# Kernel tuning notes

Measured on AMD Instinct MI355X. Metric: run time of the kernel, lower is better.

## Reference

```python
import math
import jax, jax.numpy as jnp
import numpy as np

N, B, C, H, K = 1024, 8, 512, 8, 5  # seq len, batch, d_model, heads, near_kth
NEG = -1.0e9


def setup_inputs() -> dict:
    key = jax.random.key(0)
    ks = jax.random.split(key, 10)
    s = 0.02
    return {
        "query": jax.random.normal(ks[0], (N, B, C), jnp.float32),
        "key_t": jax.random.normal(ks[1], (N, B, C), jnp.float32),
        "value": jax.random.normal(ks[2], (N, B, C), jnp.float32),
        "src_position": jax.random.normal(ks[3], (N, B, 3), jnp.float32),
        "tgt_position": jax.random.normal(ks[4], (N, B, 3), jnp.float32),
        # nn.MultiheadAttention params (in_proj split into q/k/v, plus out_proj)
        "Wq": jax.random.normal(ks[5], (C, C), jnp.float32) * s,
        "Wk": jax.random.normal(ks[6], (C, C), jnp.float32) * s,
        "Wv": jax.random.normal(ks[7], (C, C), jnp.float32) * s,
        "bq": jnp.zeros((C,), jnp.float32),
        "bk": jnp.zeros((C,), jnp.float32),
        "bv": jnp.zeros((C,), jnp.float32),
        "Wo": jax.random.normal(ks[8], (C, C), jnp.float32) * s,
        "bo": jnp.zeros((C,), jnp.float32),
    }


def reference(query, key_t, value, src_position, tgt_position,
              Wq, Wk, Wv, bq, bk, bv, Wo, bo):
    # --- 'nearby' positional mask ---------------------------------------
    # dist[b, tgt, src] = ||src_position[src,b] - tgt_position[tgt,b]||^2
    diff = src_position[None, :, :, :] - tgt_position[:, None, :, :]  # (Nt,Ns,B,3)
    dist = jnp.sum(diff * diff, axis=-1).transpose(2, 0, 1)           # (B,Nt,Ns)
    # torch: topk(dist, k=5, dim=1, largest=False) -> 5 nearest TARGETS per source
    _, idx = jax.lax.top_k(-dist.transpose(0, 2, 1), K)               # (B,Ns,K) tgt idx
    mask = jnp.full((B, N, N), NEG, jnp.float32)
    b_i = jnp.arange(B)[:, None, None]
    s_i = jnp.arange(N)[None, :, None]
    mask = mask.at[b_i, idx, s_i].set(0.0)                            # (B,Nt,Ns)

    # --- multihead attention (eval mode, dropout=0) ----------------------
    hd = C // H
    scale = 1.0 / math.sqrt(hd)
    q = ((query @ Wq.T + bq) * scale).reshape(N, B, H, hd)
    k = (key_t @ Wk.T + bk).reshape(N, B, H, hd)
    v = (value @ Wv.T + bv).reshape(N, B, H, hd)
    scores = jnp.einsum('tbhd,sbhd->bhts', q, k) + mask[:, None]      # (B,H,Nt,Ns)
    attn = jax.nn.softmax(scores, axis=-1)
    ctx = jnp.einsum('bhts,sbhd->tbhd', attn, v).reshape(N, B, C)
    out = ctx @ Wo.T + bo                                             # (N,B,C)
    attn_avg = attn.mean(axis=1)                                      # (B,Nt,Ns)
    return out, attn_avg
```

## Files before the change

kernel.cpp:

```cpp
#include <hip/hip_runtime.h>
#include <cstdint>
#include <cstddef>

#define NSEQ 1024
#define BATCH 8
#define CMODEL 512
#define NHEAD 8
#define HDIM 64
#define CAP 64
#define FLTMAX 3.402823466e+38f

typedef short bf16x8 __attribute__((ext_vector_type(8)));
typedef float f32x4 __attribute__((ext_vector_type(4)));
typedef unsigned short ushort8v __attribute__((ext_vector_type(8)));
typedef unsigned short ushort2v __attribute__((ext_vector_type(2)));

__device__ inline unsigned short f2bf(float f) {
    unsigned int u = __builtin_bit_cast(unsigned int, f);
    u += 0x7fffu + ((u >> 16) & 1u);
    return (unsigned short)(u >> 16);
}
__device__ inline float bf2f(unsigned short u) {
    return __builtin_bit_cast(float, (unsigned int)u << 16);
}

#define GLDS16(gsrc, ldst) \
    __builtin_amdgcn_global_load_lds((const __attribute__((address_space(1))) void*)(gsrc), \
                                     (__attribute__((address_space(3))) void*)(ldst), 16, 0, 0)

__global__ __launch_bounds__(256) void prep(const float* __restrict__ w0,
                                            const float* __restrict__ w1,
                                            const float* __restrict__ w2,
                                            const float* __restrict__ w3,
                                            const float* __restrict__ value,
                                            unsigned short* __restrict__ o0,
                                            unsigned short* __restrict__ o1,
                                            unsigned short* __restrict__ o2,
                                            unsigned short* __restrict__ o3,
                                            unsigned int* __restrict__ zp,
                                            float* __restrict__ vm_raw) {
    const int bid = blockIdx.x;
    const int tid = threadIdx.x;
    if (bid < 512) {
        const int idx = bid * 256 + tid;
        const int seg = idx >> 15;
        const int c   = idx & 32767;
        const float* src = seg == 0 ? w0 : seg == 1 ? w1 : seg == 2 ? w2 : w3;
        unsigned short* dst = seg == 0 ? o0 : seg == 1 ? o1 : seg == 2 ? o2 : o3;
        const float4 v0 = *(const float4*)(src + (size_t)c * 8);
        const float4 v1 = *(const float4*)(src + (size_t)c * 8 + 4);
        ushort8v u;
        u[0] = f2bf(v0.x); u[1] = f2bf(v0.y); u[2] = f2bf(v0.z); u[3] = f2bf(v0.w);
        u[4] = f2bf(v1.x); u[5] = f2bf(v1.y); u[6] = f2bf(v1.z); u[7] = f2bf(v1.w);
        *(ushort8v*)(dst + (size_t)c * 8) = u;
        return;
    }
    if (bid < 544) {
        zp[(bid - 512) * 256 + tid] = 0u;
        return;
    }
    const int cb = bid - 544;
    const int b = cb >> 3, cg = cb & 7;
    const int ts = tid >> 6, c = cg * 64 + (tid & 63);
    float s = 0.f;
    for (int i = 0; i < 256; ++i) {
        const int t = ts * 256 + i;
        s += value[((size_t)t * BATCH + b) * CMODEL + c];
    }
    __shared__ float sh[4][64];
    sh[ts][tid & 63] = s;
    __syncthreads();
    if (ts == 0)
        vm_raw[b * CMODEL + c] = sh[0][tid & 63] + sh[1][tid & 63] +
                                 sh[2][tid & 63] + sh[3][tid & 63];
}

__global__ __launch_bounds__(256) void topk_scatter(const float* __restrict__ srcp,
                                                    const float* __restrict__ tgtp,
                                                    int* __restrict__ row_cnt,
                                                    int* __restrict__ row_list,
                                                    const unsigned short* __restrict__ Wv,
                                                    const float* __restrict__ bv,
                                                    const float* __restrict__ vm_raw,
                                                    float* __restrict__ vm) {
    if (blockIdx.x >= 2048) {
        const int bsel = blockIdx.x - 2048;
        const int c0 = threadIdx.x * 2;
        float s0 = 0.f, s1 = 0.f;
        const unsigned short* w0r = Wv + (size_t)c0 * CMODEL;
        const unsigned short* w1r = w0r + CMODEL;
        const float* vr = vm_raw + bsel * CMODEL;
        for (int k = 0; k < CMODEL; ++k) {
            const float v = vr[k];
            s0 += v * bf2f(w0r[k]);
            s1 += v * bf2f(w1r[k]);
        }
        vm[bsel * CMODEL + c0]     = s0 * (1.f / (float)NSEQ) + bv[c0];
        vm[bsel * CMODEL + c0 + 1] = s1 * (1.f / (float)NSEQ) + bv[c0 + 1];
        return;
    }

    const int w = threadIdx.x >> 6, lane = threadIdx.x & 63;
    const int wg = blockIdx.x * 4 + w;
    const int s = wg & 1023, b = wg >> 10;

    const float sx = srcp[((size_t)s * BATCH + b) * 3 + 0];
    const float sy = srcp[((size_t)s * BATCH + b) * 3 + 1];
    const float sz = srcp[((size_t)s * BATCH + b) * 3 + 2];

    float dv[16];
    #pragma unroll
    for (int i = 0; i < 16; ++i) {
        const int t = i * 64 + lane;
        const float dx = tgtp[((size_t)t * BATCH + b) * 3 + 0] - sx;
        const float dy = tgtp[((size_t)t * BATCH + b) * 3 + 1] - sy;
        const float dz = tgtp[((size_t)t * BATCH + b) * 3 + 2] - sz;
        dv[i] = dx * dx + dy * dy + dz * dz;
    }

    #pragma unroll
    for (int k = 0; k < 5; ++k) {
        float bvv = FLTMAX;
        int   bii = 0x7fffffff;
        #pragma unroll
        for (int i = 0; i < 16; ++i) {
            if (dv[i] < bvv) { bvv = dv[i]; bii = i * 64 + lane; }
        }
        #pragma unroll
        for (int off = 1; off < 64; off <<= 1) {
            const float ov = __shfl_xor(bvv, off);
            const int   oi = __shfl_xor(bii, off);
            if (ov < bvv || (ov == bvv && oi < bii)) { bvv = ov; bii = oi; }
        }
        if (lane == (bii & 63)) {
            #pragma unroll
            for (int i = 0; i < 16; ++i)
                if (bii == i * 64 + lane) dv[i] = FLTMAX;
        }
        if (lane == 0) {
            const int pos = atomicAdd(&row_cnt[b * NSEQ + bii], 1);
            if (pos < CAP) row_list[((size_t)b * NSEQ + bii) * CAP + pos] = s;
        }
    }
}

__device__ inline void gemm_fp32A_body(const float* __restrict__ A,
                                       const unsigned short* __restrict__ Wbf,
                                       const float* __restrict__ bias,
                                       unsigned short* __restrict__ outp,
                                       float scale, int m0, int n0) {
    __shared__ __align__(16) unsigned short smem[3 * 8192];
    const int tid = threadIdx.x;
    const int l = tid & 63, w = tid >> 6;
    const int wr = (w >> 1) * 64, wc = (w & 1) * 64;
    const int lr = l & 15, g = l >> 4;

    f32x4 acc[4][4] = {};

    const int rowA = tid >> 2;
    const int slA  = tid & 3;
    const int sw   = (rowA >> 1) & 3;
    const float* aS0 = A + (size_t)(m0 + rowA) * CMODEL + slA * 8;
    const float* aS1 = aS0 + (size_t)64 * CMODEL;
    const int adst0 = rowA * 32 + (slA ^ sw) * 8;
    const int adst1 = adst0 + 64 * 32;
    const unsigned short* bS0 = Wbf + (size_t)(n0 + rowA) * CMODEL + (slA ^ sw) * 8;
    const unsigned short* bS1 = bS0 + (size_t)64 * CMODEL;
    const int wb = w * 512;

    float4 a0, a1, a2, a3;
    auto LOADA = [&](int k0) {
        a0 = *(const float4*)(aS0 + k0); a1 = *(const float4*)(aS0 + k0 + 4);
        a2 = *(const float4*)(aS1 + k0); a3 = *(const float4*)(aS1 + k0 + 4);
    };
    auto CVT_WRITE = [&](int buf) {
        ushort8v u0, u1;
        u0[0] = f2bf(a0.x); u0[1] = f2bf(a0.y); u0[2] = f2bf(a0.z); u0[3] = f2bf(a0.w);
        u0[4] = f2bf(a1.x); u0[5] = f2bf(a1.y); u0[6] = f2bf(a1.z); u0[7] = f2bf(a1.w);
        u1[0] = f2bf(a2.x); u1[1] = f2bf(a2.y); u1[2] = f2bf(a2.z); u1[3] = f2bf(a2.w);
        u1[4] = f2bf(a3.x); u1[5] = f2bf(a3.y); u1[6] = f2bf(a3.z); u1[7] = f2bf(a3.w);
        unsigned short* bb = smem + buf * 8192;
        *(ushort8v*)(bb + adst0) = u0;
        *(ushort8v*)(bb + adst1) = u1;
    };
    auto STAGE_B = [&](int k0, int buf) {
        unsigned short* bb = smem + buf * 8192 + 4096;
        GLDS16(bS0 + k0, bb + wb);
        GLDS16(bS1 + k0, bb + 2048 + wb);
    };
    auto COMPUTE = [&](const unsigned short* base) {
        bf16x8 af[4], bg[4];
        #pragma unroll
        for (int i = 0; i < 4; ++i) {
            const int ra = wr + i * 16 + lr;
            af[i] = *(const bf16x8*)(base + ra * 32 + ((g ^ ((ra >> 1) & 3)) << 3));
        }
        #pragma unroll
        for (int j = 0; j < 4; ++j) {
            const int rb = wc + j * 16 + lr;
            bg[j] = *(const bf16x8*)(base + 4096 + rb * 32 + ((g ^ ((rb >> 1) & 3)) << 3));
        }
        __builtin_amdgcn_s_setprio(1);
        #pragma unroll
        for (int i = 0; i < 4; ++i)
            #pragma unroll
            for (int j = 0; j < 4; ++j)
                acc[i][j] = __builtin_amdgcn_mfma_f32_16x16x32_bf16(af[i], bg[j], acc[i][j], 0, 0, 0);
        __builtin_amdgcn_s_setprio(0);
    };

    LOADA(0);
    STAGE_B(0, 0);
    CVT_WRITE(0);
    LOADA(32);
    STAGE_B(32, 1);

    for (int t = 0; t < 16; ++t) {
        const int cur = t % 3;
        if (t < 15) {
            CVT_WRITE((t + 1) % 3);
        } else {
            asm volatile("s_waitcnt vmcnt(0)" ::: "memory");
        }
        asm volatile("s_waitcnt lgkmcnt(0)" ::: "memory");
        __builtin_amdgcn_sched_barrier(0);
        __builtin_amdgcn_s_barrier();
        if (t < 14) {
            LOADA((t + 2) * 32);
            STAGE_B((t + 2) * 32, (t + 2) % 3);
        }
        COMPUTE(smem + cur * 8192);
    }

    #pragma unroll
    for (int i = 0; i < 4; ++i) {
        #pragma unroll
        for (int j = 0; j < 4; ++j) {
            const int col = n0 + wc + j * 16 + lr;
            const float bcol = bias[col];
            #pragma unroll
            for (int r = 0; r < 4; ++r) {
                const int row = m0 + wr + i * 16 + g * 4 + r;
                const float val = (acc[i][j][r] + bcol) * scale;
                const int t = row >> 3, bb = row & 7;
                outp[((size_t)(bb * NSEQ + t)) * CMODEL + col] = f2bf(val);
            }
        }
    }
}

__global__ __launch_bounds__(256, 3) void gemm_proj(const float* __restrict__ Aq,
                                                    const float* __restrict__ Ak,
                                                    const float* __restrict__ Av,
                                                    const unsigned short* __restrict__ Wq,
                                                    const unsigned short* __restrict__ Wk,
                                                    const unsigned short* __restrict__ Wv,
                                                    const float* __restrict__ bq,
                                                    const float* __restrict__ bk,
                                                    const float* __restrict__ bv,
                                                    unsigned short* __restrict__ oq,
                                                    unsigned short* __restrict__ ok,
                                                    unsigned short* __restrict__ ov) {
    const int p = blockIdx.x;
    const int logical = (p & 7) * 96 + (p >> 3);
    const int z = logical >> 8;
    const int r = logical & 255;
    const int m0 = (r >> 2) * 128, n0 = (r & 3) * 128;
    const float* A = z == 0 ? Aq : z == 1 ? Ak : Av;
    const unsigned short* W = z == 0 ? Wq : z == 1 ? Wk : Wv;
    const float* bi = z == 0 ? bq : z == 1 ? bk : bv;
    unsigned short* o = z == 0 ? oq : z == 1 ? ok : ov;
    const float sc = z == 0 ? 0.125f : 1.0f;
    gemm_fp32A_body(A, W, bi, o, sc, m0, n0);
}

__global__ __launch_bounds__(256, 3) void gemm_out(const unsigned short* __restrict__ Abf,
                                                   const unsigned short* __restrict__ Wbf,
                                                   const float* __restrict__ bias,
                                                   float* __restrict__ out) {
    __shared__ __align__(16) unsigned short smem[3 * 8192];
    const int p = blockIdx.x;
    const int logical = (p & 7) * 32 + (p >> 3);
    const int m0 = (logical >> 2) * 128, n0 = (logical & 3) * 128;

    const int tid = threadIdx.x;
    const int l = tid & 63, w = tid >> 6;
    const int wr = (w >> 1) * 64, wc = (w & 1) * 64;
    const int lr = l & 15, g = l >> 4;

    f32x4 acc[4][4] = {};

    const int rowX = tid >> 2;
    const int kg0  = (tid & 3) ^ ((rowX >> 1) & 3);
    const unsigned short* aS0 = Abf + (size_t)(m0 + rowX) * CMODEL + kg0 * 8;
    const unsigned short* aS1 = aS0 + (size_t)64 * CMODEL;
    const unsigned short* bS0 = Wbf + (size_t)(n0 + rowX) * CMODEL + kg0 * 8;
    const unsigned short* bS1 = bS0 + (size_t)64 * CMODEL;
    const int wb = w * 512;

    auto STAGE = [&](int k0, int buf) {
        unsigned short* bb = smem + buf * 8192;
        GLDS16(aS0 + k0, bb + wb);
        GLDS16(aS1 + k0, bb + 2048 + wb);
        GLDS16(bS0 + k0, bb + 4096 + wb);
        GLDS16(bS1 + k0, bb + 6144 + wb);
    };
    auto COMPUTE = [&](const unsigned short* base) {
        bf16x8 af[4], bg[4];
        #pragma unroll
        for (int i = 0; i < 4; ++i) {
            const int ra = wr + i * 16 + lr;
            af[i] = *(const bf16x8*)(base + ra * 32 + ((g ^ ((ra >> 1) & 3)) << 3));
        }
        #pragma unroll
        for (int j = 0; j < 4; ++j) {
            const int rb = wc + j * 16 + lr;
            bg[j] = *(const bf16x8*)(base + 4096 + rb * 32 + ((g ^ ((rb >> 1) & 3)) << 3));
        }
        __builtin_amdgcn_s_setprio(1);
        #pragma unroll
        for (int i = 0; i < 4; ++i)
            #pragma unroll
            for (int j = 0; j < 4; ++j)
                acc[i][j] = __builtin_amdgcn_mfma_f32_16x16x32_bf16(af[i], bg[j], acc[i][j], 0, 0, 0);
        __builtin_amdgcn_s_setprio(0);
    };

    STAGE(0, 0);
    STAGE(32, 1);

    int cur = 0;
    for (int t = 0; t < 15; ++t) {
        asm volatile("s_waitcnt vmcnt(4)" ::: "memory");
        __builtin_amdgcn_s_barrier();
        if (t < 14) {
            int nb = cur + 2; if (nb >= 3) nb -= 3;
            STAGE((t + 2) * 32, nb);
        }
        COMPUTE(smem + cur * 8192);
        ++cur; if (cur == 3) cur = 0;
    }
    asm volatile("s_waitcnt vmcnt(0)" ::: "memory");
    __builtin_amdgcn_s_barrier();
    COMPUTE(smem + cur * 8192);

    #pragma unroll
    for (int i = 0; i < 4; ++i) {
        #pragma unroll
        for (int j = 0; j < 4; ++j) {
            const int col = n0 + wc + j * 16 + lr;
            const float bcol = bias[col];
            #pragma unroll
            for (int r = 0; r < 4; ++r) {
                const int row = m0 + wr + i * 16 + g * 4 + r;
                out[(size_t)row * CMODEL + col] = acc[i][j][r] + bcol;
            }
        }
    }
}

__global__ __launch_bounds__(256) void sparse_attn(const unsigned short* __restrict__ q_ws,
                                                   const unsigned short* __restrict__ k_ws,
                                                   const unsigned short* __restrict__ v_ws,
                                                   const int* __restrict__ row_cnt,
                                                   const int* __restrict__ row_list,
                                                   const float* __restrict__ vm,
                                                   unsigned short* __restrict__ ctx,
                                                   float* __restrict__ attn_out) {
    const int t = blockIdx.x;
    const int b = blockIdx.y;
    const int tid = threadIdx.x;

    int cnt = row_cnt[b * NSEQ + t];
    if (cnt > CAP) cnt = CAP;

    float* arow = attn_out + ((size_t)b * NSEQ + t) * NSEQ;

    if (cnt == 0) {
        const float u = 1.f / (float)NSEQ;
        const float4 uv = {u, u, u, u};
        ((float4*)arow)[tid] = uv;
        for (int c = tid; c < CMODEL; c += 256)
            ctx[((size_t)t * BATCH + b) * CMODEL + c] = f2bf(vm[b * CMODEL + c]);
        return;
    }

    {
        const float4 zv = {0.f, 0.f, 0.f, 0.f};
        ((float4*)arow)[tid] = zv;
    }

    __shared__ float qs[CMODEL];
    __shared__ float esc[CAP][8];
    __shared__ float denom[8];
    __shared__ int   slist[CAP];

    if (tid < 8) denom[tid] = 0.f;
    if (tid < cnt) slist[tid] = row_list[((size_t)b * NSEQ + t) * CAP + tid];
    {
        const ushort2v qv = *(const ushort2v*)(q_ws + ((size_t)b * NSEQ + t) * CMODEL + tid * 2);
        qs[tid * 2] = bf2f(qv[0]); qs[tid * 2 + 1] = bf2f(qv[1]);
    }
    __syncthreads();

    const int wid = tid >> 6, lane = tid & 63;
    for (int i = wid; i < cnt; i += 4) {
        const int s = slist[i];
        const ushort8v kv = *(const ushort8v*)(k_ws + ((size_t)b * NSEQ + s) * CMODEL + lane * 8);
        const float* qrow = qs + lane * 8;
        float part = 0.f;
        #pragma unroll
        for (int j = 0; j < 8; ++j) part += qrow[j] * bf2f(kv[j]);
        part += __shfl_xor(part, 1);
        part += __shfl_xor(part, 2);
        part += __shfl_xor(part, 4);
        if ((lane & 7) == 0) {
            const int h = lane >> 3;
            const float e = __expf(part);
            esc[i][h] = e;
            atomicAdd(&denom[h], e);
        }
    }
    __syncthreads();

    for (int x = tid; x < cnt * 8; x += 256)
        esc[x >> 3][x & 7] /= denom[x & 7];
    __syncthreads();

    for (int i = tid; i < cnt; i += 256) {
        float pm = 0.f;
        #pragma unroll
        for (int h = 0; h < 8; ++h) pm += esc[i][h];
        arow[slist[i]] = pm * 0.125f;
    }

    const int c0 = tid * 2;
    const int h0 = c0 >> 6;
    float acc0 = 0.f, acc1 = 0.f;
    for (int i = 0; i < cnt; ++i) {
        const int s = slist[i];
        const float p = esc[i][h0];
        const ushort2v vv = *(const ushort2v*)(v_ws + ((size_t)b * NSEQ + s) * CMODEL + c0);
        acc0 += p * bf2f(vv[0]); acc1 += p * bf2f(vv[1]);
    }
    unsigned short* crow = ctx + ((size_t)t * BATCH + b) * CMODEL;
    ushort2v cv; cv[0] = f2bf(acc0); cv[1] = f2bf(acc1);
    *(ushort2v*)(crow + c0) = cv;
}

extern "C" void kernel_launch(void* const* d_in, const int* in_sizes, int n_in,
                              void* d_out, int out_size, void* d_ws, size_t ws_size,
                              hipStream_t stream) {
    (void)in_sizes; (void)n_in; (void)out_size; (void)ws_size;

    const float* query = (const float*)d_in[0];
    const float* key_t = (const float*)d_in[1];
    const float* value = (const float*)d_in[2];
    const float* srcp  = (const float*)d_in[3];
    const float* tgtp  = (const float*)d_in[4];
    const float* Wq    = (const float*)d_in[5];
    const float* Wk    = (const float*)d_in[6];
    const float* Wv    = (const float*)d_in[7];
    const float* bq    = (const float*)d_in[8];
    const float* bk    = (const float*)d_in[9];
    const float* bv    = (const float*)d_in[10];
    const float* Wo    = (const float*)d_in[11];
    const float* bo    = (const float*)d_in[12];

    float* out      = (float*)d_out;
    float* attn_out = out + (size_t)NSEQ * BATCH * CMODEL;

    const size_t NBC = (size_t)BATCH * NSEQ * CMODEL;
    const size_t WSZ = (size_t)CMODEL * CMODEL;
    unsigned short* q_ws  = (unsigned short*)d_ws;
    unsigned short* k_ws  = q_ws + NBC;
    unsigned short* v_ws  = k_ws + NBC;
    unsigned short* ctxbf = v_ws + NBC;
    unsigned short* wqbf  = ctxbf + NBC;
    unsigned short* wkbf  = wqbf + WSZ;
    unsigned short* wvbf  = wkbf + WSZ;
    unsigned short* wobf  = wvbf + WSZ;
    int*   row_cnt  = (int*)(wobf + WSZ);
    float* vm       = (float*)(row_cnt + BATCH * NSEQ);
    float* vm_raw   = vm + BATCH * CMODEL;
    int*   row_list = (int*)(vm_raw + BATCH * CMODEL);

    prep<<<608, 256, 0, stream>>>(Wq, Wk, Wv, Wo, value,
                                  wqbf, wkbf, wvbf, wobf,
                                  (unsigned int*)row_cnt, vm_raw);

    topk_scatter<<<2056, 256, 0, stream>>>(srcp, tgtp, row_cnt, row_list,
                                           wvbf, bv, vm_raw, vm);

    gemm_proj<<<768, 256, 0, stream>>>(query, key_t, value,
                                       wqbf, wkbf, wvbf,
                                       bq, bk, bv,
                                       q_ws, k_ws, v_ws);

    sparse_attn<<<dim3(NSEQ, BATCH), 256, 0, stream>>>(q_ws, k_ws, v_ws, row_cnt,
                                                       row_list, vm, ctxbf, attn_out);

    gemm_out<<<256, 256, 0, stream>>>(ctxbf, wobf, bo, out);
}
```

Before: 103.1 us.

## Transpose positions to SoA, vectorize vm GEMV, deepen gemm_proj A-load pipeline

Adds a prep pass that transposes target/source positions into structure-of-arrays buffers so top-k distance loads are coalesced. Vectorizes the per-batch value-mean GEMV with 16-byte loads. Restructures the fp32-A projection GEMM into a fully unrolled pipeline that keeps two register sets of A loads in flight, with explicit vmcnt waits. Also drops the setprio hints around the MFMA blocks. Extra workspace and register pressure are the trade-offs.

```diff
diff --git a/kernel.cpp b/kernel.cpp
--- a/kernel.cpp
+++ b/kernel.cpp
@@ -33,12 +33,16 @@
                                             const float* __restrict__ w2,
                                             const float* __restrict__ w3,
                                             const float* __restrict__ value,
+                                            const float* __restrict__ tgtp,
+                                            const float* __restrict__ srcp,
                                             unsigned short* __restrict__ o0,
                                             unsigned short* __restrict__ o1,
                                             unsigned short* __restrict__ o2,
                                             unsigned short* __restrict__ o3,
                                             unsigned int* __restrict__ zp,
-                                            float* __restrict__ vm_raw) {
+                                            float* __restrict__ vm_raw,
+                                            float* __restrict__ tgt_soa,
+                                            float* __restrict__ src_soa) {
     const int bid = blockIdx.x;
     const int tid = threadIdx.x;
     if (bid < 512) {
@@ -59,24 +63,37 @@
         zp[(bid - 512) * 256 + tid] = 0u;
         return;
     }
-    const int cb = bid - 544;
-    const int b = cb >> 3, cg = cb & 7;
-    const int ts = tid >> 6, c = cg * 64 + (tid & 63);
-    float s = 0.f;
-    for (int i = 0; i < 256; ++i) {
-        const int t = ts * 256 + i;
-        s += value[((size_t)t * BATCH + b) * CMODEL + c];
-    }
-    __shared__ float sh[4][64];
-    sh[ts][tid & 63] = s;
-    __syncthreads();
-    if (ts == 0)
-        vm_raw[b * CMODEL + c] = sh[0][tid & 63] + sh[1][tid & 63] +
-                                 sh[2][tid & 63] + sh[3][tid & 63];
-}
-
-__global__ __launch_bounds__(256) void topk_scatter(const float* __restrict__ srcp,
-                                                    const float* __restrict__ tgtp,
+    if (bid < 608) {
+        const int cb = bid - 544;
+        const int b = cb >> 3, cg = cb & 7;
+        const int ts = tid >> 6, c = cg * 64 + (tid & 63);
+        float s = 0.f;
+        for (int i = 0; i < 256; ++i) {
+            const int t = ts * 256 + i;
+            s += value[((size_t)t * BATCH + b) * CMODEL + c];
+        }
+        __shared__ float sh[4][64];
+        sh[ts][tid & 63] = s;
+        __syncthreads();
+        if (ts == 0)
+            vm_raw[b * CMODEL + c] = sh[0][tid & 63] + sh[1][tid & 63] +
+                                     sh[2][tid & 63] + sh[3][tid & 63];
+        return;
+    }
+    const int tb = bid - 608;
+    const int which = tb >> 3, b = tb & 7;
+    const float* src = which == 0 ? tgtp : srcp;
+    float* dst = which == 0 ? tgt_soa : src_soa;
+    for (int t = tid; t < NSEQ; t += 256) {
+        const float* p = src + ((size_t)t * BATCH + b) * 3;
+        dst[(b * 3 + 0) * NSEQ + t] = p[0];
+        dst[(b * 3 + 1) * NSEQ + t] = p[1];
+        dst[(b * 3 + 2) * NSEQ + t] = p[2];
+    }
+}
+
+__global__ __launch_bounds__(256) void topk_scatter(const float* __restrict__ src_soa,
+                                                    const float* __restrict__ tgt_soa,
                                                     int* __restrict__ row_cnt,
                                                     int* __restrict__ row_list,
                                                     const unsigned short* __restrict__ Wv,
@@ -90,10 +107,15 @@
         const unsigned short* w0r = Wv + (size_t)c0 * CMODEL;
         const unsigned short* w1r = w0r + CMODEL;
         const float* vr = vm_raw + bsel * CMODEL;
-        for (int k = 0; k < CMODEL; ++k) {
-            const float v = vr[k];
-            s0 += v * bf2f(w0r[k]);
-            s1 += v * bf2f(w1r[k]);
+        for (int k8 = 0; k8 < 64; ++k8) {
+            const ushort8v w0 = *(const ushort8v*)(w0r + k8 * 8);
+            const ushort8v w1 = *(const ushort8v*)(w1r + k8 * 8);
+            const float4 va = *(const float4*)(vr + k8 * 8);
+            const float4 vb = *(const float4*)(vr + k8 * 8 + 4);
+            s0 += va.x * bf2f(w0[0]) + va.y * bf2f(w0[1]) + va.z * bf2f(w0[2]) + va.w * bf2f(w0[3])
+                + vb.x * bf2f(w0[4]) + vb.y * bf2f(w0[5]) + vb.z * bf2f(w0[6]) + vb.w * bf2f(w0[7]);
+            s1 += va.x * bf2f(w1[0]) + va.y * bf2f(w1[1]) + va.z * bf2f(w1[2]) + va.w * bf2f(w1[3])
+                + vb.x * bf2f(w1[4]) + vb.y * bf2f(w1[5]) + vb.z * bf2f(w1[6]) + vb.w * bf2f(w1[7]);
         }
         vm[bsel * CMODEL + c0]     = s0 * (1.f / (float)NSEQ) + bv[c0];
         vm[bsel * CMODEL + c0 + 1] = s1 * (1.f / (float)NSEQ) + bv[c0 + 1];
@@ -104,17 +126,20 @@
     const int wg = blockIdx.x * 4 + w;
     const int s = wg & 1023, b = wg >> 10;
 
-    const float sx = srcp[((size_t)s * BATCH + b) * 3 + 0];
-    const float sy = srcp[((size_t)s * BATCH + b) * 3 + 1];
-    const float sz = srcp[((size_t)s * BATCH + b) * 3 + 2];
+    const float* tx = tgt_soa + (b * 3 + 0) * NSEQ;
+    const float* ty = tgt_soa + (b * 3 + 1) * NSEQ;
+    const float* tz = tgt_soa + (b * 3 + 2) * NSEQ;
+    const float sx = src_soa[(b * 3 + 0) * NSEQ + s];
+    const float sy = src_soa[(b * 3 + 1) * NSEQ + s];
+    const float sz = src_soa[(b * 3 + 2) * NSEQ + s];
 
     float dv[16];
     #pragma unroll
     for (int i = 0; i < 16; ++i) {
         const int t = i * 64 + lane;
-        const float dx = tgtp[((size_t)t * BATCH + b) * 3 + 0] - sx;
-        const float dy = tgtp[((size_t)t * BATCH + b) * 3 + 1] - sy;
-        const float dz = tgtp[((size_t)t * BATCH + b) * 3 + 2] - sz;
+        const float dx = tx[t] - sx;
+        const float dy = ty[t] - sy;
+        const float dz = tz[t] - sz;
         dv[i] = dx * dx + dy * dy + dz * dz;
     }
 
@@ -168,17 +193,24 @@
     const unsigned short* bS1 = bS0 + (size_t)64 * CMODEL;
     const int wb = w * 512;
 
-    float4 a0, a1, a2, a3;
-    auto LOADA = [&](int k0) {
-        a0 = *(const float4*)(aS0 + k0); a1 = *(const float4*)(aS0 + k0 + 4);
-        a2 = *(const float4*)(aS1 + k0); a3 = *(const float4*)(aS1 + k0 + 4);
+    float4 sets[2][4];
+
+    auto LOADA = [&](int S, int k0) {
+        sets[S][0] = *(const float4*)(aS0 + k0);
+        sets[S][1] = *(const float4*)(aS0 + k0 + 4);
+        sets[S][2] = *(const float4*)(aS1 + k0);
+        sets[S][3] = *(const float4*)(aS1 + k0 + 4);
     };
-    auto CVT_WRITE = [&](int buf) {
+    auto CVT_WRITE = [&](int S, int buf) {
         ushort8v u0, u1;
-        u0[0] = f2bf(a0.x); u0[1] = f2bf(a0.y); u0[2] = f2bf(a0.z); u0[3] = f2bf(a0.w);
-        u0[4] = f2bf(a1.x); u0[5] = f2bf(a1.y); u0[6] = f2bf(a1.z); u0[7] = f2bf(a1.w);
-        u1[0] = f2bf(a2.x); u1[1] = f2bf(a2.y); u1[2] = f2bf(a2.z); u1[3] = f2bf(a2.w);
-        u1[4] = f2bf(a3.x); u1[5] = f2bf(a3.y); u1[6] = f2bf(a3.z); u1[7] = f2bf(a3.w);
+        u0[0] = f2bf(sets[S][0].x); u0[1] = f2bf(sets[S][0].y);
+        u0[2] = f2bf(sets[S][0].z); u0[3] = f2bf(sets[S][0].w);
+        u0[4] = f2bf(sets[S][1].x); u0[5] = f2bf(sets[S][1].y);
+        u0[6] = f2bf(sets[S][1].z); u0[7] = f2bf(sets[S][1].w);
+        u1[0] = f2bf(sets[S][2].x); u1[1] = f2bf(sets[S][2].y);
+        u1[2] = f2bf(sets[S][2].z); u1[3] = f2bf(sets[S][2].w);
+        u1[4] = f2bf(sets[S][3].x); u1[5] = f2bf(sets[S][3].y);
+        u1[6] = f2bf(sets[S][3].z); u1[7] = f2bf(sets[S][3].w);
         unsigned short* bb = smem + buf * 8192;
         *(ushort8v*)(bb + adst0) = u0;
         *(ushort8v*)(bb + adst1) = u1;
@@ -200,37 +232,46 @@
             const int rb = wc + j * 16 + lr;
             bg[j] = *(const bf16x8*)(base + 4096 + rb * 32 + ((g ^ ((rb >> 1) & 3)) << 3));
         }
-        __builtin_amdgcn_s_setprio(1);
         #pragma unroll
         for (int i = 0; i < 4; ++i)
             #pragma unroll
             for (int j = 0; j < 4; ++j)
                 acc[i][j] = __builtin_amdgcn_mfma_f32_16x16x32_bf16(af[i], bg[j], acc[i][j], 0, 0, 0);
-        __builtin_amdgcn_s_setprio(0);
     };
 
-    LOADA(0);
+    LOADA(0, 0);
+    LOADA(1, 32);
     STAGE_B(0, 0);
-    CVT_WRITE(0);
-    LOADA(32);
     STAGE_B(32, 1);
-
-    for (int t = 0; t < 16; ++t) {
-        const int cur = t % 3;
-        if (t < 15) {
-            CVT_WRITE((t + 1) % 3);
-        } else {
-            asm volatile("s_waitcnt vmcnt(0)" ::: "memory");
-        }
+    CVT_WRITE(0, 0);
+    LOADA(0, 64);
+
+    #pragma unroll
+    for (int t = 0; t < 13; ++t) {
+        const int S = (t + 1) & 1;
+        CVT_WRITE(S, (t + 1) % 3);
+        LOADA(S, (t + 3) * 32);
+        asm volatile("s_waitcnt vmcnt(10)" ::: "memory");
         asm volatile("s_waitcnt lgkmcnt(0)" ::: "memory");
-        __builtin_amdgcn_sched_barrier(0);
         __builtin_amdgcn_s_barrier();
-        if (t < 14) {
-            LOADA((t + 2) * 32);
-            STAGE_B((t + 2) * 32, (t + 2) % 3);
-        }
-        COMPUTE(smem + cur * 8192);
-    }
+        STAGE_B((t + 2) * 32, (t + 2) % 3);
+        COMPUTE(smem + (t % 3) * 8192);
+    }
+    CVT_WRITE(0, 2);
+    asm volatile("s_waitcnt vmcnt(6)" ::: "memory");
+    asm volatile("s_waitcnt lgkmcnt(0)" ::: "memory");
+    __builtin_amdgcn_s_barrier();
+    STAGE_B(15 * 32, 0);
+    COMPUTE(smem + 1 * 8192);
+    CVT_WRITE(1, 0);
+    asm volatile("s_waitcnt vmcnt(2)" ::: "memory");
+    asm volatile("s_waitcnt lgkmcnt(0)" ::: "memory");
+    __builtin_amdgcn_s_barrier();
+    COMPUTE(smem + 2 * 8192);
+    asm volatile("s_waitcnt vmcnt(0)" ::: "memory");
+    asm volatile("s_waitcnt lgkmcnt(0)" ::: "memory");
+    __builtin_amdgcn_s_barrier();
+    COMPUTE(smem + 0 * 8192);
 
     #pragma unroll
     for (int i = 0; i < 4; ++i) {
@@ -317,13 +358,11 @@
             const int rb = wc + j * 16 + lr;
             bg[j] = *(const bf16x8*)(base + 4096 + rb * 32 + ((g ^ ((rb >> 1) & 3)) << 3));
         }
-        __builtin_amdgcn_s_setprio(1);
         #pragma unroll
         for (int i = 0; i < 4; ++i)
             #pragma unroll
             for (int j = 0; j < 4; ++j)
                 acc[i][j] = __builtin_amdgcn_mfma_f32_16x16x32_bf16(af[i], bg[j], acc[i][j], 0, 0, 0);
-        __builtin_amdgcn_s_setprio(0);
     };
 
     STAGE(0, 0);
@@ -483,13 +522,16 @@
     int*   row_cnt  = (int*)(wobf + WSZ);
     float* vm       = (float*)(row_cnt + BATCH * NSEQ);
     float* vm_raw   = vm + BATCH * CMODEL;
-    int*   row_list = (int*)(vm_raw + BATCH * CMODEL);
-
-    prep<<<608, 256, 0, stream>>>(Wq, Wk, Wv, Wo, value,
+    float* tgt_soa  = vm_raw + BATCH * CMODEL;
+    float* src_soa  = tgt_soa + (size_t)BATCH * 3 * NSEQ;
+    int*   row_list = (int*)(src_soa + (size_t)BATCH * 3 * NSEQ);
+
+    prep<<<624, 256, 0, stream>>>(Wq, Wk, Wv, Wo, value, tgtp, srcp,
                                   wqbf, wkbf, wvbf, wobf,
-                                  (unsigned int*)row_cnt, vm_raw);
-
-    topk_scatter<<<2056, 256, 0, stream>>>(srcp, tgtp, row_cnt, row_list,
+                                  (unsigned int*)row_cnt, vm_raw,
+                                  tgt_soa, src_soa);
+
+    topk_scatter<<<2056, 256, 0, stream>>>(src_soa, tgt_soa, row_cnt, row_list,
                                            wvbf, bv, vm_raw, vm);
 
     gemm_proj<<<768, 256, 0, stream>>>(query, key_t, value,
```

New measurement: 95.98 us. 1.07x faster.
